# Kernel optimization log

Measured on AMD Instinct MI355X. Metric: run time of the kernel, lower is better.

## Reference

```python
import math
import jax, jax.numpy as jnp
import numpy as np

B, L, D, H = 4, 2048, 512, 8
DK = D // H  # d_keys = d_values = 64
KFAC = 3


def setup_inputs() -> dict:
    key = jax.random.key(0)
    ks = jax.random.split(key, 10)
    u_part = min(KFAC * int(math.ceil(math.log(L))), L)  # 24
    scale = 1.0 / math.sqrt(D)
    return {
        "queries": jax.random.normal(ks[0], (B, L, D), jnp.float32),
        "keys": jax.random.normal(ks[1], (B, L, D), jnp.float32),
        "values": jax.random.normal(ks[2], (B, L, D), jnp.float32),
        "index_sample": jax.random.randint(ks[3], (L, u_part), 0, L, jnp.int32),
        "Wq": jax.random.normal(ks[4], (D, D), jnp.float32) * scale,
        "bq": jnp.zeros((D,), jnp.float32),
        "Wk": jax.random.normal(ks[5], (D, D), jnp.float32) * scale,
        "bk": jnp.zeros((D,), jnp.float32),
        "Wv": jax.random.normal(ks[6], (D, D), jnp.float32) * scale,
        "bv": jnp.zeros((D,), jnp.float32),
        "Wo": jax.random.normal(ks[7], (D, D), jnp.float32) * scale,
        "bo": jnp.zeros((D,), jnp.float32),
    }


def reference(queries, keys, values, index_sample, Wq, bq, Wk, bk, Wv, bv, Wo, bo):
    b, q_len, d_out = queries.shape
    k_len = keys.shape[1]
    # projections -> [B, H, L, DK]
    q = (queries @ Wq + bq).reshape(b, q_len, H, DK).transpose(0, 2, 1, 3)
    k = (keys @ Wk + bk).reshape(b, k_len, H, DK).transpose(0, 2, 1, 3)
    v = (values @ Wv + bv).reshape(b, k_len, H, DK).transpose(0, 2, 1, 3)

    n_top = min(KFAC * int(math.ceil(math.log(q_len))), q_len)  # u

    # --- _prob_qk: sampled QK scores to pick sparse queries ---
    # k_sample: [B, H, q_len, sample_k, DK]
    k_sample = k[:, :, index_sample, :]
    q_k_sample = jnp.einsum("bhld,bhlsd->bhls", q, k_sample)
    m = jnp.max(q_k_sample, axis=-1) - jnp.sum(q_k_sample, axis=-1) / k_len
    _, m_top = jax.lax.top_k(m, n_top)  # [B, H, u]

    q_reduce = jnp.take_along_axis(q, m_top[..., None], axis=2)  # [B, H, u, DK]
    scores_top = jnp.einsum("bhud,bhkd->bhuk", q_reduce, k) / math.sqrt(d_out)

    # --- masked (causal) branch: mask_flag=True ---
    causal = jnp.triu(jnp.ones((q_len, k_len), bool), 1)
    indicator = causal[m_top]  # [B, H, u, k_len]
    scores_top = jnp.where(indicator, -jnp.inf, scores_top)

    attn = jax.nn.softmax(scores_top, axis=-1)  # [B, H, u, k_len]
    context = jnp.cumsum(v, axis=2)  # default context for non-selected queries
    attn_values = jnp.einsum("bhuk,bhkd->bhud", attn, v)

    bidx = jnp.arange(b)[:, None, None]
    hidx = jnp.arange(H)[None, :, None]
    context = context.at[bidx, hidx, m_top].set(attn_values)

    # mix=False: transpose back to [B, L, H, DV] then merge heads
    context = context.transpose(0, 2, 1, 3).reshape(b, q_len, H * DK)
    out = context @ Wo + bo  # dropout_rate=0 / inference: identity
    return out
```

## Files before the change

kernel.cpp:

```cpp
#include <hip/hip_runtime.h>
#include <hip/hip_bf16.h>
#include <math.h>

#define Bq 4
#define Lq 2048
#define Dq 512
#define Hq 8
#define DKq 64
#define Uq 24
#define TSCAN 16
#define NTILE (Lq / TSCAN)
#define JCH 256
#define NCH (Lq / JCH)
#define TKCH 8

typedef unsigned short ushort_t;
typedef unsigned long long u64;
typedef __attribute__((ext_vector_type(8))) short bfrag8;
typedef __attribute__((ext_vector_type(4))) float facc4;

__device__ inline ushort_t bf16_rne(float f) {
  unsigned u = __float_as_uint(f);
  u += 0x7FFF + ((u >> 16) & 1);
  return (ushort_t)(u >> 16);
}
__device__ inline float bf16f(ushort_t h) {
  return __uint_as_float(((unsigned)h) << 16);
}
__device__ inline unsigned fkey(float f) {
  unsigned u = __float_as_uint(f);
  return (u & 0x80000000u) ? ~u : (u | 0x80000000u);
}
__device__ __forceinline__ void gl2lds16(const void* g, void* l) {
  __builtin_amdgcn_global_load_lds(
      (const __attribute__((address_space(1))) unsigned*)g,
      (__attribute__((address_space(3))) unsigned*)l, 16, 0, 0);
}

__global__ __launch_bounds__(256) void prep_all(
    const float* __restrict__ xq, const float* __restrict__ xk,
    const float* __restrict__ xv, ushort_t* __restrict__ qh,
    ushort_t* __restrict__ ql, ushort_t* __restrict__ kh,
    ushort_t* __restrict__ kl, ushort_t* __restrict__ vh,
    const float* __restrict__ W0, const float* __restrict__ W1,
    const float* __restrict__ W2, const float* __restrict__ W3,
    ushort_t* __restrict__ T0h, ushort_t* __restrict__ T0l,
    ushort_t* __restrict__ T1h, ushort_t* __restrict__ T1l,
    ushort_t* __restrict__ T2h, ushort_t* __restrict__ T3h) {
  __shared__ float tile[32][33];
  int y = blockIdx.y;
  if (y < 3) {
    const float* x = y == 0 ? xq : (y == 1 ? xk : xv);
    ushort_t* hi = y == 0 ? qh : (y == 1 ? kh : vh);
    ushort_t* lo = y == 0 ? ql : kl;
    int t = blockIdx.x * 256 + threadIdx.x;
    float4 v = *(const float4*)&x[(size_t)t * 4];
    ushort_t h0 = bf16_rne(v.x), h1 = bf16_rne(v.y), h2 = bf16_rne(v.z),
             h3 = bf16_rne(v.w);
    ushort4 hh = {h0, h1, h2, h3};
    *(ushort4*)&hi[(size_t)t * 4] = hh;
    if (y < 2) {
      ushort4 ll = {bf16_rne(v.x - bf16f(h0)), bf16_rne(v.y - bf16f(h1)),
                    bf16_rne(v.z - bf16f(h2)), bf16_rne(v.w - bf16f(h3))};
      *(ushort4*)&lo[(size_t)t * 4] = ll;
    }
    return;
  }
  int id = blockIdx.x;
  if (id >= 1024) return;
  int z = id >> 8;
  const float* W = z == 0 ? W0 : (z == 1 ? W1 : (z == 2 ? W2 : W3));
  ushort_t* Th = z == 0 ? T0h : (z == 1 ? T1h : (z == 2 ? T2h : T3h));
  ushort_t* Tl = z == 0 ? T0l : (z == 1 ? T1l : nullptr);
  int k0 = ((id >> 4) & 15) * 32, n0 = (id & 15) * 32;
  int tx = threadIdx.x & 31, ty = threadIdx.x >> 5;
  for (int r = ty; r < 32; r += 8)
    tile[tx][r] = W[(size_t)(k0 + r) * 512 + n0 + tx];
  __syncthreads();
  for (int r = ty; r < 32; r += 8) {
    float v = tile[r][tx];
    ushort_t h = bf16_rne(v);
    Th[(size_t)(n0 + r) * 512 + k0 + tx] = h;
    if (Tl) Tl[(size_t)(n0 + r) * 512 + k0 + tx] = bf16_rne(v - bf16f(h));
  }
}

__global__ __launch_bounds__(256) void gemm_qkv(
    const ushort_t* __restrict__ Aqh, const ushort_t* __restrict__ Aql,
    const ushort_t* __restrict__ Akh, const ushort_t* __restrict__ Akl,
    const ushort_t* __restrict__ Avh,
    const ushort_t* __restrict__ Wqh, const ushort_t* __restrict__ Wql,
    const ushort_t* __restrict__ Wkh, const ushort_t* __restrict__ Wkl,
    const ushort_t* __restrict__ Wvh,
    const float* __restrict__ bq, const float* __restrict__ bk,
    const float* __restrict__ bv,
    float* __restrict__ qo, float* __restrict__ ko, float* __restrict__ vo) {
  __shared__ ushort_t Ash[128][32], Asl[128][32];
  __shared__ ushort_t Bsh[128][32], Bsl[128][32];
  int which = blockIdx.z;
  const ushort_t* Ah = which == 0 ? Aqh : (which == 1 ? Akh : Avh);
  const ushort_t* Al = which == 0 ? Aql : Akl;
  const ushort_t* Bh = which == 0 ? Wqh : (which == 1 ? Wkh : Wvh);
  const ushort_t* Bl = which == 0 ? Wql : Wkl;
  const float* bias = which == 0 ? bq : (which == 1 ? bk : bv);
  float* C = which == 0 ? qo : (which == 1 ? ko : vo);
  const bool split = which < 2;

  int bm = blockIdx.x, bn = blockIdx.y;
  int tid = threadIdx.x;
  int wave = tid >> 6, lane = tid & 63;
  int wm = (wave & 1) * 64, wn = (wave >> 1) * 64;
  int quad = lane >> 4, lm = lane & 15;
  int srow = tid >> 2;
  int slc = (((tid & 3) ^ ((tid >> 3) & 3))) * 8;
  int sphys = (tid & 3) * 8;
  int rsw = (quad ^ ((lm >> 1) & 3)) * 8;
  facc4 acc[4][4] = {};

  for (int k0 = 0; k0 < 512; k0 += 32) {
#pragma unroll
    for (int p = 0; p < 2; ++p) {
      int row = srow + p * 64;
      size_t ga = (size_t)(bm * 128 + row) * 512 + k0 + slc;
      size_t gb = (size_t)(bn * 128 + row) * 512 + k0 + slc;
      gl2lds16(&Ah[ga], &Ash[row][sphys]);
      gl2lds16(&Bh[gb], &Bsh[row][sphys]);
      if (split) {
        gl2lds16(&Al[ga], &Asl[row][sphys]);
        gl2lds16(&Bl[gb], &Bsl[row][sphys]);
      }
    }
    __syncthreads();
    bfrag8 afh[4], afl[4], bfh[4], bfl[4];
#pragma unroll
    for (int mt = 0; mt < 4; ++mt) {
      afh[mt] = *(bfrag8*)&Ash[wm + mt * 16 + lm][rsw];
      if (split) afl[mt] = *(bfrag8*)&Asl[wm + mt * 16 + lm][rsw];
    }
#pragma unroll
    for (int nt = 0; nt < 4; ++nt) {
      bfh[nt] = *(bfrag8*)&Bsh[wn + nt * 16 + lm][rsw];
      if (split) bfl[nt] = *(bfrag8*)&Bsl[wn + nt * 16 + lm][rsw];
    }
#pragma unroll
    for (int mt = 0; mt < 4; ++mt)
#pragma unroll
      for (int nt = 0; nt < 4; ++nt) {
        facc4 a = acc[mt][nt];
        a = __builtin_amdgcn_mfma_f32_16x16x32_bf16(afh[mt], bfh[nt], a, 0, 0, 0);
        if (split) {
          a = __builtin_amdgcn_mfma_f32_16x16x32_bf16(afl[mt], bfh[nt], a, 0, 0, 0);
          a = __builtin_amdgcn_mfma_f32_16x16x32_bf16(afh[mt], bfl[nt], a, 0, 0, 0);
        }
        acc[mt][nt] = a;
      }
    __syncthreads();
  }
#pragma unroll
  for (int mt = 0; mt < 4; ++mt)
#pragma unroll
    for (int nt = 0; nt < 4; ++nt) {
      int col = bn * 128 + wn + nt * 16 + lm;
      float bv2 = bias[col];
#pragma unroll
      for (int r = 0; r < 4; ++r) {
        int row = bm * 128 + wm + mt * 16 + quad * 4 + r;
        C[(size_t)row * 512 + col] = acc[mt][nt][r] + bv2;
      }
    }
}

__global__ __launch_bounds__(256) void gemm_bf16(
    const ushort_t* __restrict__ A, const ushort_t* __restrict__ Bt,
    const float* __restrict__ bias, float* __restrict__ C) {
  __shared__ ushort_t As[128][32];
  __shared__ ushort_t Bs[128][32];
  int bm = blockIdx.x, bn = blockIdx.y;
  int tid = threadIdx.x;
  int wave = tid >> 6, lane = tid & 63;
  int wm = (wave & 1) * 64, wn = (wave >> 1) * 64;
  int quad = lane >> 4, lm = lane & 15;
  int srow = tid >> 2;
  int slc = (((tid & 3) ^ ((tid >> 3) & 3))) * 8;
  int sphys = (tid & 3) * 8;
  int rsw = (quad ^ ((lm >> 1) & 3)) * 8;
  facc4 acc[4][4] = {};

  for (int k0 = 0; k0 < 512; k0 += 32) {
#pragma unroll
    for (int p = 0; p < 2; ++p) {
      int row = srow + p * 64;
      gl2lds16(&A[(size_t)(bm * 128 + row) * 512 + k0 + slc], &As[row][sphys]);
      gl2lds16(&Bt[(size_t)(bn * 128 + row) * 512 + k0 + slc], &Bs[row][sphys]);
    }
    __syncthreads();
    bfrag8 af[4], bf[4];
#pragma unroll
    for (int mt = 0; mt < 4; ++mt)
      af[mt] = *(bfrag8*)&As[wm + mt * 16 + lm][rsw];
#pragma unroll
    for (int nt = 0; nt < 4; ++nt)
      bf[nt] = *(bfrag8*)&Bs[wn + nt * 16 + lm][rsw];
#pragma unroll
    for (int mt = 0; mt < 4; ++mt)
#pragma unroll
      for (int nt = 0; nt < 4; ++nt)
        acc[mt][nt] = __builtin_amdgcn_mfma_f32_16x16x32_bf16(
            af[mt], bf[nt], acc[mt][nt], 0, 0, 0);
    __syncthreads();
  }
#pragma unroll
  for (int mt = 0; mt < 4; ++mt)
#pragma unroll
    for (int nt = 0; nt < 4; ++nt) {
      int col = bn * 128 + wn + nt * 16 + lm;
      float bv = bias[col];
#pragma unroll
      for (int r = 0; r < 4; ++r) {
        int row = bm * 128 + wm + mt * 16 + quad * 4 + r;
        C[(size_t)row * 512 + col] = acc[mt][nt][r] + bv;
      }
    }
}

__global__ __launch_bounds__(256) void compute_m(
    const float* __restrict__ q, const float* __restrict__ k,
    const int* __restrict__ idxs, float* __restrict__ m) {
  int wave = threadIdx.x >> 6, lane = threadIdx.x & 63;
  int lq = lane >> 4, dq = lane & 15;
  int slot = (blockIdx.x * 4 + wave) * 4 + lq;
  int l = slot & (Lq - 1);
  int bh = slot >> 11;
  int h = bh & (Hq - 1), b = bh >> 3;
  float4 qv = *(const float4*)&q[((size_t)b * Lq + l) * Dq + h * DKq + dq * 4];
  const float* kb = &k[(size_t)b * Lq * Dq + h * DKq + dq * 4];
  const int* ib = &idxs[l * Uq];
  float mx = -INFINITY, sm = 0.f;
#pragma unroll
  for (int s = 0; s < Uq; ++s) {
    int j = ib[s];
    float4 kv = *(const float4*)&kb[(size_t)j * Dq];
    float p = qv.x * kv.x + qv.y * kv.y + qv.z * kv.z + qv.w * kv.w;
    p += __shfl_xor(p, 1, 64);
    p += __shfl_xor(p, 2, 64);
    p += __shfl_xor(p, 4, 64);
    p += __shfl_xor(p, 8, 64);
    mx = fmaxf(mx, p);
    sm += p;
  }
  if (dq == 0) m[slot] = mx - sm * (1.0f / Lq);
}

__global__ __launch_bounds__(256) void topk_fused(
    const float* __restrict__ m, int* __restrict__ mtop,
    int* __restrict__ repl) {
  __shared__ u64 red[2][4];
  __shared__ int mt[Uq];
  int bh = blockIdx.x;
  int tid = threadIdx.x, wave = tid >> 6, lane = tid & 63;
  u64 keys[TKCH];
#pragma unroll
  for (int c = 0; c < TKCH; ++c) {
    int gidx = c * 256 + tid;
    float v = m[(size_t)bh * Lq + gidx];
    keys[c] = ((u64)fkey(v) << 32) | (u64)(Lq - 1 - gidx);
  }
#pragma unroll 1
  for (int it = 0; it < Uq; ++it) {
    u64 lb = keys[0];
#pragma unroll
    for (int c = 1; c < TKCH; ++c) lb = keys[c] > lb ? keys[c] : lb;
#pragma unroll
    for (int off = 32; off; off >>= 1) {
      u64 o = __shfl_xor(lb, off, 64);
      lb = o > lb ? o : lb;
    }
    int p = it & 1;
    if (lane == 0) red[p][wave] = lb;
    __syncthreads();
    u64 w0 = red[p][0] > red[p][1] ? red[p][0] : red[p][1];
    u64 w1 = red[p][2] > red[p][3] ? red[p][2] : red[p][3];
    u64 win = w0 > w1 ? w0 : w1;
    if (tid == 0) {
      int idx = Lq - 1 - (int)(win & 0xFFFFFFFFull);
      mtop[bh * Uq + it] = idx;
      mt[it] = idx;
    }
#pragma unroll
    for (int c = 0; c < TKCH; ++c)
      if (keys[c] == win) keys[c] = 0;
  }
  __syncthreads();
  int* rb = &repl[(size_t)bh * Lq];
#pragma unroll
  for (int c = 0; c < TKCH; ++c) rb[c * 256 + tid] = -1;
  __syncthreads();
  if (tid < Uq) rb[mt[tid]] = tid;
}

#define JT 256
#define JS 64

__global__ __launch_bounds__(256) void scores_kernel(
    const float* __restrict__ q, const float* __restrict__ k,
    const int* __restrict__ mtop, float* __restrict__ scg) {
  __shared__ float qs[Uq][DKq + 1];
  __shared__ float ks[JS][DKq + 1];
  __shared__ int i0s[Uq];
  int bh = blockIdx.y;
  int jt = blockIdx.x;
  int h = bh & (Hq - 1);
  int b = bh >> 3;
  int tid = threadIdx.x;
  if (tid < Uq) i0s[tid] = mtop[bh * Uq + tid];
  __syncthreads();
  for (int s = tid; s < Uq * 16; s += 256) {
    int u = s >> 4, qd = (s & 15) * 4;
    float4 t = *(const float4*)&q[((size_t)b * Lq + i0s[u]) * Dq + h * DKq + qd];
    qs[u][qd] = t.x; qs[u][qd + 1] = t.y; qs[u][qd + 2] = t.z; qs[u][qd + 3] = t.w;
  }
  int jp = tid & 31;
  int ug = tid >> 5;
  const float scale = 0.044194173824159216f;
  for (int sub = 0; sub < JT / JS; ++sub) {
    int jbase = jt * JT + sub * JS;
    __syncthreads();
    for (int s = tid; s < JS * 16; s += 256) {
      int j = s >> 4, qd = (s & 15) * 4;
      float4 t = *(const float4*)&k[((size_t)b * Lq + jbase + j) * Dq + h * DKq + qd];
      ks[j][qd] = t.x; ks[j][qd + 1] = t.y; ks[j][qd + 2] = t.z; ks[j][qd + 3] = t.w;
    }
    __syncthreads();
    float acc[3][2] = {};
    int j0 = jp * 2, j1 = j0 + 1;
#pragma unroll 8
    for (int d = 0; d < DKq; ++d) {
      float k0 = ks[j0][d], k1 = ks[j1][d];
#pragma unroll
      for (int uu = 0; uu < 3; ++uu) {
        float qv = qs[ug * 3 + uu][d];
        acc[uu][0] += qv * k0;
        acc[uu][1] += qv * k1;
      }
    }
#pragma unroll
    for (int uu = 0; uu < 3; ++uu) {
      int u = ug * 3 + uu;
      scg[((size_t)(bh * Uq + u)) * Lq + jbase + j0] = acc[uu][0] * scale;
      scg[((size_t)(bh * Uq + u)) * Lq + jbase + j1] = acc[uu][1] * scale;
    }
  }
}

__global__ __launch_bounds__(256) void softmax_pv_partial(
    const float* __restrict__ scg, const float* __restrict__ v,
    const int* __restrict__ mtop, float* __restrict__ pmax,
    float* __restrict__ psum, float* __restrict__ pvp) {
  int blk = blockIdx.y;
  int jc = blockIdx.x;
  int bh = blk / Uq;
  int h = bh & (Hq - 1);
  int b = bh >> 3;
  int n = mtop[blk] + 1;
  int j0 = jc * JCH;
  if (j0 >= n) return;
  int cnt = min(JCH, n - j0);
  int tid = threadIdx.x, wave = tid >> 6, lane = tid & 63;
  __shared__ float es[JCH];
  __shared__ float red[4][DKq];
  __shared__ float rr[4];

  const float* row = &scg[(size_t)blk * Lq + j0];
  float mx = (tid < cnt) ? row[tid] : -INFINITY;
#pragma unroll
  for (int off = 32; off; off >>= 1) mx = fmaxf(mx, __shfl_xor(mx, off, 64));
  if (lane == 0) rr[wave] = mx;
  __syncthreads();
  mx = fmaxf(fmaxf(rr[0], rr[1]), fmaxf(rr[2], rr[3]));
  __syncthreads();

  float e = (tid < cnt) ? __expf(row[tid] - mx) : 0.f;
  es[tid] = e;
  float sm = e;
#pragma unroll
  for (int off = 32; off; off >>= 1) sm += __shfl_xor(sm, off, 64);
  if (lane == 0) rr[wave] = sm;
  __syncthreads();

  float acc = 0.f;
  const float* vb = &v[((size_t)b * Lq + j0) * Dq + h * DKq + lane];
  int jlo = wave * 64;
  int jhi = min(jlo + 64, cnt);
#pragma unroll 4
  for (int j = jlo; j < jhi; ++j) acc += es[j] * vb[(size_t)j * Dq];
  red[wave][lane] = acc;
  __syncthreads();
  if (wave == 0) {
    if (lane == 0) {
      pmax[blk * NCH + jc] = mx;
      psum[blk * NCH + jc] = rr[0] + rr[1] + rr[2] + rr[3];
    }
    pvp[((size_t)blk * NCH + jc) * DKq + lane] =
        red[0][lane] + red[1][lane] + red[2][lane] + red[3][lane];
  }
}

__global__ __launch_bounds__(128) void tile_sum(const float* __restrict__ v,
                                                float* __restrict__ tsum) {
  int blk = blockIdx.x;
  int tile = blk & (NTILE - 1);
  int b = blk >> 7;
  int d4 = threadIdx.x;
  float4 s = {0.f, 0.f, 0.f, 0.f};
  const float* base = &v[((size_t)b * Lq + tile * TSCAN) * Dq + d4 * 4];
#pragma unroll
  for (int r = 0; r < TSCAN; ++r) {
    float4 x = *(const float4*)&base[(size_t)r * Dq];
    s.x += x.x; s.y += x.y; s.z += x.z; s.w += x.w;
  }
  *(float4*)&tsum[((size_t)b * NTILE + tile) * Dq + d4 * 4] = s;
}

__global__ __launch_bounds__(128) void build_context(
    const float* __restrict__ v, const float* __restrict__ tsum,
    const int* __restrict__ repl,
    const float* __restrict__ pmax, const float* __restrict__ psum,
    const float* __restrict__ pvp, ushort_t* __restrict__ ctxh) {
  int blk = blockIdx.x;
  int tile = blk & (NTILE - 1);
  int b = blk >> 7;
  int d4 = threadIdx.x;
  int h = d4 >> 4;
  float4 run = {0.f, 0.f, 0.f, 0.f};
  const float* tb = &tsum[(size_t)b * NTILE * Dq + d4 * 4];
#pragma unroll 4
  for (int t = 0; t < tile; ++t) {
    float4 x = *(const float4*)&tb[(size_t)t * Dq];
    run.x += x.x; run.y += x.y; run.z += x.z; run.w += x.w;
  }
  const int* replb = &repl[(size_t)(b * Hq + h) * Lq + tile * TSCAN];
  const float* vb = &v[((size_t)b * Lq + tile * TSCAN) * Dq + d4 * 4];
  ushort_t* cb = &ctxh[((size_t)b * Lq + tile * TSCAN) * Dq + d4 * 4];
#pragma unroll
  for (int r = 0; r < TSCAN; ++r) {
    float4 x = *(const float4*)&vb[(size_t)r * Dq];
    run.x += x.x; run.y += x.y; run.z += x.z; run.w += x.w;
    int u = replb[r];
    float4 val = run;
    if (u >= 0) {
      int l = tile * TSCAN + r;
      int blku = (b * Hq + h) * Uq + u;
      int nc = (l + JCH) / JCH;
      float gmax = -INFINITY;
      for (int c = 0; c < nc; ++c) gmax = fmaxf(gmax, pmax[blku * NCH + c]);
      float tot = 0.f;
      float4 acc = {0.f, 0.f, 0.f, 0.f};
      for (int c = 0; c < nc; ++c) {
        float wgt = __expf(pmax[blku * NCH + c] - gmax);
        tot += psum[blku * NCH + c] * wgt;
        float4 pv = *(const float4*)&pvp[((size_t)blku * NCH + c) * DKq +
                                         (d4 & 15) * 4];
        acc.x += pv.x * wgt; acc.y += pv.y * wgt;
        acc.z += pv.z * wgt; acc.w += pv.w * wgt;
      }
      float inv = 1.0f / tot;
      val.x = acc.x * inv; val.y = acc.y * inv;
      val.z = acc.z * inv; val.w = acc.w * inv;
    }
    ushort4 o = {bf16_rne(val.x), bf16_rne(val.y), bf16_rne(val.z),
                 bf16_rne(val.w)};
    *(ushort4*)&cb[(size_t)r * Dq] = o;
  }
}

extern "C" void kernel_launch(void* const* d_in, const int* in_sizes, int n_in,
                              void* d_out, int out_size, void* d_ws,
                              size_t ws_size, hipStream_t stream) {
  const float* queries = (const float*)d_in[0];
  const float* keys    = (const float*)d_in[1];
  const float* values  = (const float*)d_in[2];
  const int*   idxs    = (const int*)d_in[3];
  const float* Wq = (const float*)d_in[4];
  const float* bq = (const float*)d_in[5];
  const float* Wk = (const float*)d_in[6];
  const float* bk = (const float*)d_in[7];
  const float* Wv = (const float*)d_in[8];
  const float* bv = (const float*)d_in[9];
  const float* Wo = (const float*)d_in[10];
  const float* bo = (const float*)d_in[11];
  float* out = (float*)d_out;

  const size_t BLD = (size_t)Bq * Lq * Dq;
  char* w = (char*)d_ws;
  float* q    = (float*)w; w += BLD * 4;
  float* k    = (float*)w; w += BLD * 4;
  float* v    = (float*)w; w += BLD * 4;
  float* scg  = (float*)w; w += (size_t)Bq * Hq * Uq * Lq * 4;
  float* m    = (float*)w; w += (size_t)Bq * Hq * Lq * 4;
  float* tsum = (float*)w; w += (size_t)Bq * NTILE * Dq * 4;
  int* mtop   = (int*)w;   w += Bq * Hq * Uq * 4;
  int* repl   = (int*)w;   w += (size_t)Bq * Hq * Lq * 4;
  float* pmax = (float*)w; w += (size_t)Bq * Hq * Uq * NCH * 4;
  float* psum = (float*)w; w += (size_t)Bq * Hq * Uq * NCH * 4;
  float* pvp  = (float*)w; w += (size_t)Bq * Hq * Uq * NCH * DKq * 4;
  ushort_t* ctxh = (ushort_t*)w; w += BLD * 2;
  ushort_t* Aqh = (ushort_t*)w; w += BLD * 2;
  ushort_t* Aql = (ushort_t*)w; w += BLD * 2;
  ushort_t* Akh = (ushort_t*)w; w += BLD * 2;
  ushort_t* Akl = (ushort_t*)w; w += BLD * 2;
  ushort_t* Avh = (ushort_t*)w; w += BLD * 2;
  const size_t WSZ = 512 * 512;
  ushort_t* Wqh = (ushort_t*)w; w += WSZ * 2;
  ushort_t* Wql = (ushort_t*)w; w += WSZ * 2;
  ushort_t* Wkh = (ushort_t*)w; w += WSZ * 2;
  ushort_t* Wkl = (ushort_t*)w; w += WSZ * 2;
  ushort_t* Wvh = (ushort_t*)w; w += WSZ * 2;
  ushort_t* Woh = (ushort_t*)w; w += WSZ * 2;

  {
    dim3 pgrid(BLD / 4 / 256, 4);
    prep_all<<<pgrid, 256, 0, stream>>>(queries, keys, values, Aqh, Aql, Akh,
                                        Akl, Avh, Wq, Wk, Wv, Wo, Wqh, Wql,
                                        Wkh, Wkl, Wvh, Woh);
  }

  {
    dim3 ggrid(64, 4, 3);
    gemm_qkv<<<ggrid, 256, 0, stream>>>(Aqh, Aql, Akh, Akl, Avh, Wqh, Wql,
                                        Wkh, Wkl, Wvh, bq, bk, bv, q, k, v);
  }

  compute_m<<<(Bq * Hq * Lq) / 16, 256, 0, stream>>>(q, k, idxs, m);
  topk_fused<<<Bq * Hq, 256, 0, stream>>>(m, mtop, repl);

  {
    dim3 sgrid(Lq / JT, Bq * Hq);
    scores_kernel<<<sgrid, 256, 0, stream>>>(q, k, mtop, scg);
  }
  {
    dim3 pgrid(NCH, Bq * Hq * Uq);
    softmax_pv_partial<<<pgrid, 256, 0, stream>>>(scg, v, mtop, pmax, psum, pvp);
  }

  tile_sum<<<Bq * NTILE, 128, 0, stream>>>(v, tsum);
  build_context<<<Bq * NTILE, 128, 0, stream>>>(v, tsum, repl, pmax, psum,
                                                pvp, ctxh);

  {
    dim3 ggrid(64, 4);
    gemm_bf16<<<ggrid, 256, 0, stream>>>(ctxh, Woh, bo, out);
  }
}
```

Before: 279.1 us.

## Fuse scores, softmax and PV; piggyback tile sums; add super-tile prefix sums

Merges the QK-scores kernel and the softmax/PV partial kernel into one attn_fused kernel. Scores stay in registers and shared memory instead of going through a global scg buffer, and chunks beyond the largest selected index are skipped. Tile sums of V are computed by extra blocks of the compute_m launch, and a new super-tile sum level is built in extra blocks of the topk launch. This lets build_context's prefix loop read at most 16+7 entries instead of up to 127. The cost is a larger shared footprint in attn_fused and fewer, bigger blocks (one per bh×256-key chunk) handling the PV work.

```diff
diff --git a/kernel.cpp b/kernel.cpp
--- a/kernel.cpp
+++ b/kernel.cpp
@@ -10,6 +10,7 @@
 #define Uq 24
 #define TSCAN 16
 #define NTILE (Lq / TSCAN)
+#define NSUP 16
 #define JCH 256
 #define NCH (Lq / JCH)
 #define TKCH 8
@@ -223,12 +224,29 @@
     }
 }
 
-__global__ __launch_bounds__(256) void compute_m(
+__global__ __launch_bounds__(256) void compute_m_tiles(
     const float* __restrict__ q, const float* __restrict__ k,
-    const int* __restrict__ idxs, float* __restrict__ m) {
+    const int* __restrict__ idxs, float* __restrict__ m,
+    const float* __restrict__ v, float* __restrict__ tsum) {
+  int bx = blockIdx.x;
+  if (bx >= 4096) {
+    int unit = (bx - 4096) * 2 + (threadIdx.x >> 7);
+    int d4 = threadIdx.x & 127;
+    int tile = unit & (NTILE - 1);
+    int b = unit >> 7;
+    float4 s = {0.f, 0.f, 0.f, 0.f};
+    const float* base = &v[((size_t)b * Lq + tile * TSCAN) * Dq + d4 * 4];
+#pragma unroll
+    for (int r = 0; r < TSCAN; ++r) {
+      float4 x = *(const float4*)&base[(size_t)r * Dq];
+      s.x += x.x; s.y += x.y; s.z += x.z; s.w += x.w;
+    }
+    *(float4*)&tsum[((size_t)b * NTILE + tile) * Dq + d4 * 4] = s;
+    return;
+  }
   int wave = threadIdx.x >> 6, lane = threadIdx.x & 63;
   int lq = lane >> 4, dq = lane & 15;
-  int slot = (blockIdx.x * 4 + wave) * 4 + lq;
+  int slot = (bx * 4 + wave) * 4 + lq;
   int l = slot & (Lq - 1);
   int bh = slot >> 11;
   int h = bh & (Hq - 1), b = bh >> 3;
@@ -251,9 +269,25 @@
   if (dq == 0) m[slot] = mx - sm * (1.0f / Lq);
 }
 
-__global__ __launch_bounds__(256) void topk_fused(
+__global__ __launch_bounds__(256) void topk_stile(
     const float* __restrict__ m, int* __restrict__ mtop,
-    int* __restrict__ repl) {
+    int* __restrict__ repl, const float* __restrict__ tsum,
+    float* __restrict__ stsum) {
+  if (blockIdx.x >= 32) {
+    int unit = (blockIdx.x - 32) * 2 + (threadIdx.x >> 7);
+    int d4 = threadIdx.x & 127;
+    int s = unit & (NSUP - 1);
+    int b = unit >> 4;
+    float4 acc = {0.f, 0.f, 0.f, 0.f};
+    const float* tb = &tsum[((size_t)b * NTILE + s * 8) * Dq + d4 * 4];
+#pragma unroll
+    for (int i = 0; i < 8; ++i) {
+      float4 t = *(const float4*)&tb[(size_t)i * Dq];
+      acc.x += t.x; acc.y += t.y; acc.z += t.z; acc.w += t.w;
+    }
+    *(float4*)&stsum[((size_t)b * NSUP + s) * Dq + d4 * 4] = acc;
+    return;
+  }
   __shared__ u64 red[2][4];
   __shared__ int mt[Uq];
   int bh = blockIdx.x;
@@ -301,19 +335,28 @@
 #define JT 256
 #define JS 64
 
-__global__ __launch_bounds__(256) void scores_kernel(
+__global__ __launch_bounds__(256) void attn_fused(
     const float* __restrict__ q, const float* __restrict__ k,
-    const int* __restrict__ mtop, float* __restrict__ scg) {
+    const float* __restrict__ v, const int* __restrict__ mtop,
+    float* __restrict__ pmax, float* __restrict__ psum,
+    float* __restrict__ pvp) {
   __shared__ float qs[Uq][DKq + 1];
   __shared__ float ks[JS][DKq + 1];
+  __shared__ float es[Uq][260];
   __shared__ int i0s[Uq];
+  int jt = blockIdx.x;
   int bh = blockIdx.y;
-  int jt = blockIdx.x;
   int h = bh & (Hq - 1);
   int b = bh >> 3;
   int tid = threadIdx.x;
   if (tid < Uq) i0s[tid] = mtop[bh * Uq + tid];
   __syncthreads();
+  int maxn = 0;
+#pragma unroll
+  for (int u2 = 0; u2 < Uq; ++u2) maxn = max(maxn, i0s[u2] + 1);
+  int jbase0 = jt * JT;
+  if (maxn <= jbase0) return;
+
   for (int s = tid; s < Uq * 16; s += 256) {
     int u = s >> 4, qd = (s & 15) * 4;
     float4 t = *(const float4*)&q[((size_t)b * Lq + i0s[u]) * Dq + h * DKq + qd];
@@ -321,109 +364,116 @@
   }
   int jp = tid & 31;
   int ug = tid >> 5;
+  float sreg[3][8] = {};
+#pragma unroll
+  for (int sub = 0; sub < 4; ++sub) {
+    int jb = jbase0 + sub * JS;
+    __syncthreads();
+    if (jb < maxn) {
+      for (int s = tid; s < JS * 16; s += 256) {
+        int j = s >> 4, qd = (s & 15) * 4;
+        float4 t =
+            *(const float4*)&k[((size_t)b * Lq + jb + j) * Dq + h * DKq + qd];
+        ks[j][qd] = t.x; ks[j][qd + 1] = t.y;
+        ks[j][qd + 2] = t.z; ks[j][qd + 3] = t.w;
+      }
+    }
+    __syncthreads();
+    if (jb < maxn) {
+      float acc[3][2] = {};
+      int j0 = jp * 2, j1 = j0 + 1;
+#pragma unroll 8
+      for (int d = 0; d < DKq; ++d) {
+        float k0 = ks[j0][d], k1 = ks[j1][d];
+#pragma unroll
+        for (int uu = 0; uu < 3; ++uu) {
+          float qv = qs[ug * 3 + uu][d];
+          acc[uu][0] += qv * k0;
+          acc[uu][1] += qv * k1;
+        }
+      }
+#pragma unroll
+      for (int uu = 0; uu < 3; ++uu) {
+        sreg[uu][sub * 2] = acc[uu][0];
+        sreg[uu][sub * 2 + 1] = acc[uu][1];
+      }
+    }
+  }
+
   const float scale = 0.044194173824159216f;
-  for (int sub = 0; sub < JT / JS; ++sub) {
-    int jbase = jt * JT + sub * JS;
-    __syncthreads();
-    for (int s = tid; s < JS * 16; s += 256) {
-      int j = s >> 4, qd = (s & 15) * 4;
-      float4 t = *(const float4*)&k[((size_t)b * Lq + jbase + j) * Dq + h * DKq + qd];
-      ks[j][qd] = t.x; ks[j][qd + 1] = t.y; ks[j][qd + 2] = t.z; ks[j][qd + 3] = t.w;
-    }
-    __syncthreads();
-    float acc[3][2] = {};
-    int j0 = jp * 2, j1 = j0 + 1;
-#pragma unroll 8
-    for (int d = 0; d < DKq; ++d) {
-      float k0 = ks[j0][d], k1 = ks[j1][d];
-#pragma unroll
-      for (int uu = 0; uu < 3; ++uu) {
-        float qv = qs[ug * 3 + uu][d];
-        acc[uu][0] += qv * k0;
-        acc[uu][1] += qv * k1;
-      }
-    }
-#pragma unroll
-    for (int uu = 0; uu < 3; ++uu) {
-      int u = ug * 3 + uu;
-      scg[((size_t)(bh * Uq + u)) * Lq + jbase + j0] = acc[uu][0] * scale;
-      scg[((size_t)(bh * Uq + u)) * Lq + jbase + j1] = acc[uu][1] * scale;
-    }
-  }
-}
-
-__global__ __launch_bounds__(256) void softmax_pv_partial(
-    const float* __restrict__ scg, const float* __restrict__ v,
-    const int* __restrict__ mtop, float* __restrict__ pmax,
-    float* __restrict__ psum, float* __restrict__ pvp) {
-  int blk = blockIdx.y;
-  int jc = blockIdx.x;
-  int bh = blk / Uq;
-  int h = bh & (Hq - 1);
-  int b = bh >> 3;
-  int n = mtop[blk] + 1;
-  int j0 = jc * JCH;
-  if (j0 >= n) return;
-  int cnt = min(JCH, n - j0);
-  int tid = threadIdx.x, wave = tid >> 6, lane = tid & 63;
-  __shared__ float es[JCH];
-  __shared__ float red[4][DKq];
-  __shared__ float rr[4];
-
-  const float* row = &scg[(size_t)blk * Lq + j0];
-  float mx = (tid < cnt) ? row[tid] : -INFINITY;
-#pragma unroll
-  for (int off = 32; off; off >>= 1) mx = fmaxf(mx, __shfl_xor(mx, off, 64));
-  if (lane == 0) rr[wave] = mx;
-  __syncthreads();
-  mx = fmaxf(fmaxf(rr[0], rr[1]), fmaxf(rr[2], rr[3]));
-  __syncthreads();
-
-  float e = (tid < cnt) ? __expf(row[tid] - mx) : 0.f;
-  es[tid] = e;
-  float sm = e;
-#pragma unroll
-  for (int off = 32; off; off >>= 1) sm += __shfl_xor(sm, off, 64);
-  if (lane == 0) rr[wave] = sm;
-  __syncthreads();
-
-  float acc = 0.f;
-  const float* vb = &v[((size_t)b * Lq + j0) * Dq + h * DKq + lane];
-  int jlo = wave * 64;
-  int jhi = min(jlo + 64, cnt);
+#pragma unroll
+  for (int uu = 0; uu < 3; ++uu) {
+    int u = ug * 3 + uu;
+    int lu = i0s[u];
+    float sv[8];
+    float mx = -INFINITY;
+#pragma unroll
+    for (int t = 0; t < 8; ++t) {
+      int jl = (t >> 1) * JS + jp * 2 + (t & 1);
+      float x = sreg[uu][t] * scale;
+      bool ok = (jbase0 + jl) <= lu;
+      x = ok ? x : -INFINITY;
+      sv[t] = x;
+      mx = fmaxf(mx, x);
+    }
+#pragma unroll
+    for (int off = 16; off; off >>= 1) mx = fmaxf(mx, __shfl_xor(mx, off, 64));
+    float sm = 0.f;
+#pragma unroll
+    for (int t = 0; t < 8; ++t) {
+      int jl = (t >> 1) * JS + jp * 2 + (t & 1);
+      float e = (sv[t] == -INFINITY) ? 0.f : __expf(sv[t] - mx);
+      es[u][jl] = e;
+      sm += e;
+    }
+#pragma unroll
+    for (int off = 16; off; off >>= 1) sm += __shfl_xor(sm, off, 64);
+    if (jp == 0) {
+      int blku = bh * Uq + u;
+      pmax[blku * NCH + jt] = mx;
+      psum[blku * NCH + jt] = sm;
+    }
+  }
+
+  int wv = tid >> 6, lane = tid & 63;
+  float a6[6] = {};
+#pragma unroll
+  for (int sub = 0; sub < 4; ++sub) {
+    int jb = jbase0 + sub * JS;
+    __syncthreads();
+    if (jb < maxn) {
+      for (int s = tid; s < JS * 16; s += 256) {
+        int j = s >> 4, qd = (s & 15) * 4;
+        float4 t =
+            *(const float4*)&v[((size_t)b * Lq + jb + j) * Dq + h * DKq + qd];
+        ks[j][qd] = t.x; ks[j][qd + 1] = t.y;
+        ks[j][qd + 2] = t.z; ks[j][qd + 3] = t.w;
+      }
+    }
+    __syncthreads();
+    if (jb < maxn) {
 #pragma unroll 4
-  for (int j = jlo; j < jhi; ++j) acc += es[j] * vb[(size_t)j * Dq];
-  red[wave][lane] = acc;
-  __syncthreads();
-  if (wave == 0) {
-    if (lane == 0) {
-      pmax[blk * NCH + jc] = mx;
-      psum[blk * NCH + jc] = rr[0] + rr[1] + rr[2] + rr[3];
-    }
-    pvp[((size_t)blk * NCH + jc) * DKq + lane] =
-        red[0][lane] + red[1][lane] + red[2][lane] + red[3][lane];
-  }
-}
-
-__global__ __launch_bounds__(128) void tile_sum(const float* __restrict__ v,
-                                                float* __restrict__ tsum) {
-  int blk = blockIdx.x;
-  int tile = blk & (NTILE - 1);
-  int b = blk >> 7;
-  int d4 = threadIdx.x;
-  float4 s = {0.f, 0.f, 0.f, 0.f};
-  const float* base = &v[((size_t)b * Lq + tile * TSCAN) * Dq + d4 * 4];
-#pragma unroll
-  for (int r = 0; r < TSCAN; ++r) {
-    float4 x = *(const float4*)&base[(size_t)r * Dq];
-    s.x += x.x; s.y += x.y; s.z += x.z; s.w += x.w;
-  }
-  *(float4*)&tsum[((size_t)b * NTILE + tile) * Dq + d4 * 4] = s;
+      for (int j = 0; j < JS; j += 4) {
+        float v0 = ks[j][lane], v1 = ks[j + 1][lane];
+        float v2 = ks[j + 2][lane], v3 = ks[j + 3][lane];
+#pragma unroll
+        for (int uu = 0; uu < 6; ++uu) {
+          float4 ee = *(const float4*)&es[wv * 6 + uu][sub * JS + j];
+          a6[uu] += ee.x * v0 + ee.y * v1 + ee.z * v2 + ee.w * v3;
+        }
+      }
+    }
+  }
+#pragma unroll
+  for (int uu = 0; uu < 6; ++uu) {
+    int blku = bh * Uq + wv * 6 + uu;
+    pvp[((size_t)blku * NCH + jt) * DKq + lane] = a6[uu];
+  }
 }
 
 __global__ __launch_bounds__(128) void build_context(
     const float* __restrict__ v, const float* __restrict__ tsum,
-    const int* __restrict__ repl,
+    const float* __restrict__ stsum, const int* __restrict__ repl,
     const float* __restrict__ pmax, const float* __restrict__ psum,
     const float* __restrict__ pvp, ushort_t* __restrict__ ctxh) {
   int blk = blockIdx.x;
@@ -431,12 +481,18 @@
   int b = blk >> 7;
   int d4 = threadIdx.x;
   int h = d4 >> 4;
+  int sup = tile >> 3;
   float4 run = {0.f, 0.f, 0.f, 0.f};
-  const float* tb = &tsum[(size_t)b * NTILE * Dq + d4 * 4];
-#pragma unroll 4
-  for (int t = 0; t < tile; ++t) {
-    float4 x = *(const float4*)&tb[(size_t)t * Dq];
-    run.x += x.x; run.y += x.y; run.z += x.z; run.w += x.w;
+  const float* sb = &stsum[(size_t)b * NSUP * Dq + d4 * 4];
+  for (int s = 0; s < sup; ++s) {
+    float4 t = *(const float4*)&sb[(size_t)s * Dq];
+    run.x += t.x; run.y += t.y; run.z += t.z; run.w += t.w;
+  }
+  const float* tb = &tsum[((size_t)b * NTILE + sup * 8) * Dq + d4 * 4];
+  int rem = tile & 7;
+  for (int i = 0; i < rem; ++i) {
+    float4 t = *(const float4*)&tb[(size_t)i * Dq];
+    run.x += t.x; run.y += t.y; run.z += t.z; run.w += t.w;
   }
   const int* replb = &repl[(size_t)(b * Hq + h) * Lq + tile * TSCAN];
   const float* vb = &v[((size_t)b * Lq + tile * TSCAN) * Dq + d4 * 4];
@@ -495,9 +551,9 @@
   float* q    = (float*)w; w += BLD * 4;
   float* k    = (float*)w; w += BLD * 4;
   float* v    = (float*)w; w += BLD * 4;
-  float* scg  = (float*)w; w += (size_t)Bq * Hq * Uq * Lq * 4;
   float* m    = (float*)w; w += (size_t)Bq * Hq * Lq * 4;
   float* tsum = (float*)w; w += (size_t)Bq * NTILE * Dq * 4;
+  float* stsum= (float*)w; w += (size_t)Bq * NSUP * Dq * 4;
   int* mtop   = (int*)w;   w += Bq * Hq * Uq * 4;
   int* repl   = (int*)w;   w += (size_t)Bq * Hq * Lq * 4;
   float* pmax = (float*)w; w += (size_t)Bq * Hq * Uq * NCH * 4;
@@ -530,21 +586,17 @@
                                         Wkh, Wkl, Wvh, bq, bk, bv, q, k, v);
   }
 
-  compute_m<<<(Bq * Hq * Lq) / 16, 256, 0, stream>>>(q, k, idxs, m);
-  topk_fused<<<Bq * Hq, 256, 0, stream>>>(m, mtop, repl);
+  compute_m_tiles<<<4096 + 256, 256, 0, stream>>>(q, k, idxs, m, v, tsum);
+
+  topk_stile<<<64, 256, 0, stream>>>(m, mtop, repl, tsum, stsum);
 
   {
-    dim3 sgrid(Lq / JT, Bq * Hq);
-    scores_kernel<<<sgrid, 256, 0, stream>>>(q, k, mtop, scg);
-  }
-  {
-    dim3 pgrid(NCH, Bq * Hq * Uq);
-    softmax_pv_partial<<<pgrid, 256, 0, stream>>>(scg, v, mtop, pmax, psum, pvp);
-  }
-
-  tile_sum<<<Bq * NTILE, 128, 0, stream>>>(v, tsum);
-  build_context<<<Bq * NTILE, 128, 0, stream>>>(v, tsum, repl, pmax, psum,
-                                                pvp, ctxh);
+    dim3 agrid(Lq / JT, Bq * Hq);
+    attn_fused<<<agrid, 256, 0, stream>>>(q, k, v, mtop, pmax, psum, pvp);
+  }
+
+  build_context<<<Bq * NTILE, 128, 0, stream>>>(v, tsum, stsum, repl, pmax,
+                                                psum, pvp, ctxh);
 
   {
     dim3 ggrid(64, 4);
```

After: 258.5 us. -7.4%, faster.
